# Kernel tuning notes

Hardware: AMD Instinct MI355X
Metric: run time of the kernel (lower is better)

Reference implementation:

```python
import jax, jax.numpy as jnp
import numpy as np

K = 3           # spatial kernel size (kernel_size[1]==kernel_size[2])
STRIDE = 1
EPS_BN = 1e-5


def unfold_replicate(t, k=K, stride=STRIDE):
    """t: (b, C, H, W) -> (b, C, k*k, H//stride, W//stride).
    Replicate-padded kxk patches, row-major window order (matches F.pad(replicate)+F.unfold)."""
    b, C, H, W = t.shape
    pad = (k - 1) // 2
    tp = jnp.pad(t, ((0, 0), (0, 0), (pad, pad), (pad, pad)), mode='edge')
    patches = [tp[:, :, di:di + H:stride, dj:dj + W:stride]
               for di in range(k) for dj in range(k)]
    return jnp.stack(patches, axis=2)


def grid_sample_3d(x, grid):
    """Trilinear grid sample, zeros padding, align_corners=True.
    x: (b,c,D,H,W); grid: (b,P,3) normalized (gx,gy,gz) -> (b,c,P)."""
    b, c, D, H, W = x.shape
    ix = (grid[..., 0] + 1.0) * 0.5 * (W - 1)
    iy = (grid[..., 1] + 1.0) * 0.5 * (H - 1)
    iz = (grid[..., 2] + 1.0) * 0.5 * (D - 1)
    x0 = jnp.floor(ix); y0 = jnp.floor(iy); z0 = jnp.floor(iz)
    fx = ix - x0; fy = iy - y0; fz = iz - z0
    x0i = x0.astype(jnp.int32); y0i = y0.astype(jnp.int32); z0i = z0.astype(jnp.int32)
    x_flat = x.reshape(b, c, D * H * W)
    gather = jax.vmap(lambda xf, idx: xf[:, idx])  # (c,N),(P) -> (c,P) per batch
    out = jnp.zeros((b, c, ix.shape[1]), dtype=x.dtype)
    for dz, wz in ((0, 1.0 - fz), (1, fz)):
        zi = z0i + dz
        for dy, wy in ((0, 1.0 - fy), (1, fy)):
            yi = y0i + dy
            for dx, wx in ((0, 1.0 - fx), (1, fx)):
                xi = x0i + dx
                valid = ((zi >= 0) & (zi < D) & (yi >= 0) & (yi < H)
                         & (xi >= 0) & (xi < W))
                idx = (jnp.clip(zi, 0, D - 1) * H + jnp.clip(yi, 0, H - 1)) * W \
                      + jnp.clip(xi, 0, W - 1)
                w = (wz * wy * wx) * valid.astype(x.dtype)
                out = out + w[:, None, :] * gather(x_flat, idx)
    return out


def gca_cost(x, dp, normal, intri):
    b, c, d, H, W = x.shape
    k2 = K * K
    h, w = H // STRIDE, W // STRIDE
    ctr = k2 // 2

    dp_unf = unfold_replicate(dp)        # (b, d, k2, h, w)
    n_unf = unfold_replicate(normal)     # (b, 3, k2, h, w)
    nx, ny, nz = n_unf[:, 0], n_unf[:, 1], n_unf[:, 2]

    fx = intri[:, 0, 0][:, None, None]; fy = intri[:, 1, 1][:, None, None]
    cx = intri[:, 0, 2][:, None, None]; cy = intri[:, 1, 2][:, None, None]
    yg, xg = jnp.meshgrid(jnp.arange(H, dtype=x.dtype),
                          jnp.arange(W, dtype=x.dtype), indexing='ij')
    posx = (xg[None] - cx) / fx          # (b, H, W) normalized camera rays
    posy = (yg[None] - cy) / fy
    pos_unf = unfold_replicate(jnp.stack([posx, posy], axis=1))  # (b,2,k2,h,w)
    pu, pv = pos_unf[:, 0], pos_unf[:, 1]
    pu_c = pu[:, ctr:ctr + 1]; pv_c = pv[:, ctr:ctr + 1]

    num = nx * pu_c + ny * pv_c + nz
    den = nx * pu + ny * pv + nz
    den = jnp.where(jnp.abs(den) < 1e-8, jnp.sign(den) * 1e-8, den)
    wgt = num / den
    wgt = jnp.where(jnp.isfinite(wgt), wgt, 1.0)   # (b, k2, h, w)

    dp_ctr = dp_unf[:, :, ctr]                      # (b, d, h, w)
    dp_prog = wgt[:, None] * dp_ctr[:, :, None]     # (b, d, k2, h, w)
    interval = dp_unf[:, 1] - dp_unf[:, 0]          # (b, k2, h, w)
    z = (dp_prog - dp_unf[:, 0][:, None]) / interval[:, None]  # (b,d,k2,h,w)

    xy = jnp.broadcast_to(jnp.stack([xg, yg], axis=0)[None], (b, 2, H, W))
    xy_unf = unfold_replicate(xy)                   # (b,2,k2,h,w)
    px = jnp.broadcast_to(xy_unf[:, 0][:, None], (b, d, k2, h, w))
    py = jnp.broadcast_to(xy_unf[:, 1][:, None], (b, d, k2, h, w))

    gx = px / ((W - 1) / 2.0) - 1.0
    gy = py / ((H - 1) / 2.0) - 1.0
    gz = z / ((d - 1) / 2.0) - 1.0
    grid = jnp.stack([gx, gy, gz], axis=-1).reshape(b, d * k2 * h * w, 3)

    samp = grid_sample_3d(x, grid)                  # (b, c, d*k2*h*w)
    samp = samp.reshape(b, c, d, k2, h, w).transpose(0, 1, 3, 2, 4, 5)
    return samp.reshape(b, c * k2, d, h, w)


def reference(x, dp, normal, intri, weight, gamma, beta):
    cost = gca_cost(x, dp, normal, intri)
    y = jax.lax.conv_general_dilated(
        cost, weight, window_strides=(1, 1, 1),
        padding=[(1, 1), (0, 0), (0, 0)],
        dimension_numbers=('NCDHW', 'OIDHW', 'NCDHW'))
    # BatchNorm3d (training-mode batch stats, biased var, eps=1e-5) + ReLU
    mean = jnp.mean(y, axis=(0, 2, 3, 4), keepdims=True)
    var = jnp.var(y, axis=(0, 2, 3, 4), keepdims=True)
    g = gamma.reshape(1, -1, 1, 1, 1)
    bta = beta.reshape(1, -1, 1, 1, 1)
    return jax.nn.relu(g * (y - mean) * jax.lax.rsqrt(var + EPS_BN) + bta)


def setup_inputs() -> dict:
    key = jax.random.key(0)
    ks = jax.random.split(key, 6)
    b, c, d, H, W = 1, 8, 32, 128, 128
    out_ch = 16
    x = jax.random.normal(ks[0], (b, c, d, H, W), dtype=jnp.float32)
    # monotone depth hypotheses per pixel (interval = dp[:,1]-dp[:,0] must be nonzero)
    planes = 425.0 + 10.0 * jnp.arange(d, dtype=jnp.float32)
    scale = 1.0 + 0.05 * jax.random.uniform(ks[1], (b, 1, H, W), dtype=jnp.float32)
    dp = planes[None, :, None, None] * scale                    # (b, d, H, W)
    # near-frontal unit normals so plane-homography weights stay well-conditioned
    nxy = 0.2 * jax.random.normal(ks[2], (b, 2, H, W), dtype=jnp.float32)
    nz = 1.0 + 0.1 * jax.random.normal(ks[3], (b, 1, H, W), dtype=jnp.float32)
    n = jnp.concatenate([nxy, nz], axis=1)
    normal = n / jnp.linalg.norm(n, axis=1, keepdims=True)
    intri = jnp.broadcast_to(
        jnp.array([[1100.0, 0.0, W / 2.0],
                   [0.0, 1100.0, H / 2.0],
                   [0.0, 0.0, 1.0]], dtype=jnp.float32), (b, 3, 3))
    weight = 0.05 * jax.random.normal(ks[4], (out_ch, c * K * K, 3, 1, 1),
                                      dtype=jnp.float32)
    gamma = jnp.ones((out_ch,), jnp.float32)
    beta = jnp.zeros((out_ch,), jnp.float32)
    return {"x": x, "dp": dp, "normal": normal, "intri": intri,
            "weight": weight, "gamma": gamma, "beta": beta}
```

## Files before the change

### kernel.cpp

```cpp
#include <hip/hip_runtime.h>
#include <math.h>

#define W_    128
#define H_    128
#define HW    16384
#define D_    32
#define C_IN  8
#define OC    16
#define NRED  524288.0f

#define SXS   36
#define SXB   1948
#define TILE  2568

typedef __attribute__((ext_vector_type(8))) short bf16x8;
typedef __attribute__((ext_vector_type(4))) float f32x4;

union FragU { uint4 u; bf16x8 h; };


__device__ __forceinline__ unsigned bf16rne(float f) {
    unsigned u = __float_as_uint(f);
    return (u + 0x7fffu + ((u >> 16) & 1u)) >> 16;
}

__device__ __forceinline__ void init_ws(int t, const float* __restrict__ wsrc,
                                        float* __restrict__ ws) {
    if (t < 32) ws[t] = 0.f;
    uint4* af = reinterpret_cast<uint4*>(ws + 64);
    for (int e = t; e < 768; e += 256) {
        int lane = e & 63, pkd = e >> 6;
        int p = pkd / 3, kd = pkd - p * 3;
        int o = lane & 15, kg = lane >> 4;
        int ch = 2 * p + (kg >> 1);
        int jb = (kg & 1) * 8;
        unsigned dw[4];
#pragma unroll
        for (int r2 = 0; r2 < 4; ++r2) {
            int j0 = jb + 2 * r2, j1 = j0 + 1;
            unsigned b0 = (j0 < 9) ? bf16rne(wsrc[(o * 72 + ch * 9 + j0) * 3 + kd]) : 0u;
            unsigned b1 = (j1 < 9) ? bf16rne(wsrc[(o * 72 + ch * 9 + j1) * 3 + kd]) : 0u;
            dw[r2] = b0 | (b1 << 16);
        }
        af[e] = make_uint4(dw[0], dw[1], dw[2], dw[3]);
    }
}

__global__ __launch_bounds__(256) void k_init(const float* __restrict__ wsrc,
                                              float* __restrict__ ws) {
    init_ws((int)threadIdx.x, wsrc, ws);
}

__global__ __launch_bounds__(256) void k_transpose(const float* __restrict__ x,
                                                   float* __restrict__ xt,
                                                   const float* __restrict__ wsrc,
                                                   float* __restrict__ ws) {
    __shared__ float tile[32 * 132];
    int bid = blockIdx.x;
    int c  = bid >> 7;
    int ry = bid & 127;
    int t  = threadIdx.x;
    if (bid == 0) init_ws(t, wsrc, ws);
    const float* src = x + c * (D_ * HW) + ry * W_;
    for (int k = 0; k < 4; ++k) {
        int e  = t * 4 + k * 1024;
        int z  = e >> 7;
        int rx = e & 127;
        float4 v = *reinterpret_cast<const float4*>(src + z * HW + rx);
        *reinterpret_cast<float4*>(&tile[z * 132 + rx]) = v;
    }
    __syncthreads();
    int rx = t >> 1;
    int zh = (t & 1) * 16;
    float* dst = xt + ((size_t)(c * HW + ry * W_ + rx)) * D_ + zh;
    for (int i = 0; i < 4; ++i) {
        float4 v;
        v.x = tile[(zh + i * 4 + 0) * 132 + rx];
        v.y = tile[(zh + i * 4 + 1) * 132 + rx];
        v.z = tile[(zh + i * 4 + 2) * 132 + rx];
        v.w = tile[(zh + i * 4 + 3) * 132 + rx];
        *reinterpret_cast<float4*>(dst + i * 4) = v;
    }
}

template <bool XT, bool YBF>
__global__ __launch_bounds__(512, 4) void k_main(const float* __restrict__ x,
                                                 const float* __restrict__ xt,
                                                 const float* __restrict__ dp,
                                                 const float* __restrict__ nrm,
                                                 const float* __restrict__ intri,
                                                 const uint4* __restrict__ afr,
                                                 float* __restrict__ out,
                                                 unsigned* __restrict__ ybf,
                                                 float* __restrict__ stats) {
    __shared__ float s_pool[2 * SXB];
    __shared__ float s_B[2 * TILE];
    __shared__ float s_wgt[144], s_dp0[144], s_inv[144];
    __shared__ float s_red[64];

    int t   = threadIdx.x;
    int bid = blockIdx.x;
    int r_row = bid >> 3;
    int rx0   = (bid & 7) * 16;

    int seg = t / 144;
    int f   = t - seg * 144;
    int spx = f >> 3;
    int zq  = f & 7;
    int srow = min(max(r_row + seg - 1, 0), H_ - 1);
    int scol = min(max(rx0 - 1 + spx, 0), W_ - 1);
    const float* gsrc     = xt + ((size_t)(srow * W_ + scol)) * D_ + zq * 4;
    const float* gsrc_raw = x + (srow * W_ + scol) + (size_t)(zq * 4) * HW;
    int sdst = 4 + (seg * 18 + spx) * SXS + zq * 4;

    float4 sv;
    if (t < 432) {
        if (XT) {
            sv = *reinterpret_cast<const float4*>(gsrc);
        } else {
            sv.x = gsrc_raw[0]; sv.y = gsrc_raw[HW];
            sv.z = gsrc_raw[2 * HW]; sv.w = gsrc_raw[3 * HW];
        }
    }

    if (t < 144) {
        int p = t / 9, j = t - p * 9;
        int jd = j / 3;
        int dy = jd - 1, dx = (j - jd * 3) - 1;
        int cpix = rx0 + p;
        int ry  = min(max(r_row + dy, 0), H_ - 1);
        int rxn = min(max(cpix + dx, 0), W_ - 1);
        int nb  = ry * W_ + rxn;
        float fx = intri[0], cx = intri[2], fy = intri[4], cy = intri[5];
        float nx = nrm[nb], ny = nrm[HW + nb], nz = nrm[2 * HW + nb];
        float pu  = ((float)rxn  - cx) / fx;
        float pv  = ((float)ry   - cy) / fy;
        float puc = ((float)cpix - cx) / fx;
        float pvc = ((float)r_row - cy) / fy;
        float num = nx * puc + ny * pvc + nz;
        float den = nx * pu + ny * pv + nz;
        if (fabsf(den) < 1e-8f)
            den = (den > 0.f) ? 1e-8f : ((den < 0.f) ? -1e-8f : 0.f);
        float w = num / den;
        if (!isfinite(w)) w = 1.0f;
        float d0  = dp[nb];
        float itv = dp[HW + nb] - d0;
        s_wgt[t] = w;
        s_dp0[t] = d0;
        s_inv[t] = 1.0f / itv;
    }
    if (t < 440) {
        int b  = t / 220;
        int rm = t - b * 220;
        int off = (rm < 4) ? rm : (4 + ((rm - 4) >> 2) * SXS + 32 + ((rm - 4) & 3));
        s_pool[b * SXB + off] = 0.f;
    }
    if (t < 16) s_B[2560 + (t >> 3) * TILE + (t & 7)] = 0.f;
    __syncthreads();
    if (t < 432) *reinterpret_cast<float4*>(&s_pool[sdst]) = sv;

    int px = t & 15;
    int d  = t >> 4;
    float dpv = dp[d * HW + r_row * W_ + rx0 + px];

    int   idx[9];
    float fza[9];
#pragma unroll
    for (int j = 0; j < 9; ++j) {
        int pj = px * 9 + j;
        int jd = j / 3;
        int jx = j - jd * 3;
        float z   = (s_wgt[pj] * dpv - s_dp0[pj]) * s_inv[pj];
        float zc  = fminf(fmaxf(z, -2.0f), 34.0f);
        float z0f = floorf(zc);
        fza[j] = zc - z0f;
        idx[j] = (jd * 18 + px + jx) * SXS + (int)z0f;
    }
    __syncthreads();

    f32x4 acc0 = {0.f, 0.f, 0.f, 0.f};
    f32x4 acc1 = {0.f, 0.f, 0.f, 0.f};
    f32x4 acc2 = {0.f, 0.f, 0.f, 0.f};
    f32x4 acc3 = {0.f, 0.f, 0.f, 0.f};

    int lane = t & 63;
    int wid  = t >> 6;
    int wb   = wid * 4;
    int grp  = lane >> 4;
    unsigned* sBu = reinterpret_cast<unsigned*>(s_B);
    int wrow = (d * 16 + px) * 5;

    for (int c = 0; c < C_IN; ++c) {
        if (c < 7 && t < 432) {
            if (XT) {
                sv = *reinterpret_cast<const float4*>(gsrc + (size_t)(c + 1) * (HW * D_));
            } else {
                const float* b = gsrc_raw + (size_t)(c + 1) * (D_ * HW);
                sv.x = b[0]; sv.y = b[HW]; sv.z = b[2 * HW]; sv.w = b[3 * HW];
            }
        }
        const float* sxp = &s_pool[(c & 1) * SXB + 4];
        float cj[9];
#pragma unroll
        for (int j = 0; j < 9; ++j) {
            float a = sxp[idx[j]];
            float b = sxp[idx[j] + 1];
            cj[j] = fmaf(fza[j], b - a, a);
        }
        unsigned dwv[5];
#pragma unroll
        for (int r2 = 0; r2 < 4; ++r2) {
            asm("v_cvt_pk_bf16_f32 %0, %1, %2"
                : "=v"(dwv[r2]) : "v"(cj[2 * r2]), "v"(cj[2 * r2 + 1]));
        }
        {
            float zz = 0.f;
            asm("v_cvt_pk_bf16_f32 %0, %1, %2"
                : "=v"(dwv[4]) : "v"(cj[8]), "v"(zz));
        }
        {
            int wo = wrow + (c & 1) * TILE;
            sBu[wo + 0] = dwv[0];
            sBu[wo + 1] = dwv[1];
            sBu[wo + 2] = dwv[2];
            sBu[wo + 3] = dwv[3];
            sBu[wo + 4] = dwv[4];
        }
        if (c < 7 && t < 432) *reinterpret_cast<float4*>(&s_pool[((c + 1) & 1) * SXB + sdst]) = sv;
        __syncthreads();

        if (c & 1) {
            int p = c >> 1;
            FragU a0, a1, a2;
            a0.u = afr[(p * 3 + 0) * 64 + lane];
            a1.u = afr[(p * 3 + 1) * 64 + lane];
            a2.u = afr[(p * 3 + 2) * 64 + lane];
            int boff = ((grp & 1) ? 4 : 0) + ((grp >> 1) ? TILE : 0);
#pragma unroll
            for (int q = 0; q < 6; ++q) {
                int db = wb - 1 + q;
                if (db < 0 || db > 31) continue;
                FragU bf;
                int base = (db * 16 + px) * 5 + boff;
                bf.u.x = sBu[base + 0];
                bf.u.y = sBu[base + 1];
                bf.u.z = sBu[base + 2];
                bf.u.w = sBu[base + 3];
                if (q - 0 >= 0 && q - 0 < 4)
                    *(q == 0 ? &acc0 : q == 1 ? &acc1 : q == 2 ? &acc2 : &acc3) =
                        __builtin_amdgcn_mfma_f32_16x16x32_bf16(a0.h, bf.h,
                            *(q == 0 ? &acc0 : q == 1 ? &acc1 : q == 2 ? &acc2 : &acc3), 0, 0, 0);
                if (q - 1 >= 0 && q - 1 < 4)
                    *(q == 1 ? &acc0 : q == 2 ? &acc1 : q == 3 ? &acc2 : &acc3) =
                        __builtin_amdgcn_mfma_f32_16x16x32_bf16(a1.h, bf.h,
                            *(q == 1 ? &acc0 : q == 2 ? &acc1 : q == 3 ? &acc2 : &acc3), 0, 0, 0);
                if (q - 2 >= 0 && q - 2 < 4)
                    *(q == 2 ? &acc0 : q == 3 ? &acc1 : q == 4 ? &acc2 : &acc3) =
                        __builtin_amdgcn_mfma_f32_16x16x32_bf16(a2.h, bf.h,
                            *(q == 2 ? &acc0 : q == 3 ? &acc1 : q == 4 ? &acc2 : &acc3), 0, 0, 0);
            }
            __syncthreads();
        }
    }

    float* s_b = s_pool;
    float bns[4], bnq[4];
    int o_l = t >> 7;
    int dd  = (t >> 2) & 31;
    int q4  = t & 3;
#pragma unroll
    for (int oo = 0; oo < 4; ++oo) {
        if (grp == oo) {
#pragma unroll
            for (int r2 = 0; r2 < 4; ++r2) {
                s_b[(r2 * 32 + wb + 0) * 17 + px] = acc0[r2];
                s_b[(r2 * 32 + wb + 1) * 17 + px] = acc1[r2];
                s_b[(r2 * 32 + wb + 2) * 17 + px] = acc2[r2];
                s_b[(r2 * 32 + wb + 3) * 17 + px] = acc3[r2];
            }
        }
        __syncthreads();
        const float* brow = &s_b[(o_l * 32 + dd) * 17 + q4 * 4];
        float4 yv;
        yv.x = brow[0]; yv.y = brow[1]; yv.z = brow[2]; yv.w = brow[3];
        int o = oo * 4 + o_l;
        size_t base = (size_t)(o * 32 + dd) * HW + r_row * W_ + rx0 + q4 * 4;
        if (YBF) {
            unsigned dA, dB;
            asm("v_cvt_pk_bf16_f32 %0, %1, %2" : "=v"(dA) : "v"(yv.x), "v"(yv.y));
            asm("v_cvt_pk_bf16_f32 %0, %1, %2" : "=v"(dB) : "v"(yv.z), "v"(yv.w));
            uint2 wv; wv.x = dA; wv.y = dB;
            reinterpret_cast<uint2*>(ybf)[base >> 2] = wv;
        } else {
            *reinterpret_cast<float4*>(out + base) = yv;
        }
        bns[oo] = yv.x + yv.y + yv.z + yv.w;
        bnq[oo] = yv.x * yv.x + yv.y * yv.y + yv.z * yv.z + yv.w * yv.w;
        __syncthreads();
    }

#pragma unroll
    for (int oo = 0; oo < 4; ++oo) {
        float s = bns[oo], sq = bnq[oo];
#pragma unroll
        for (int m = 1; m < 64; m <<= 1) {
            s  += __shfl_xor(s, m, 64);
            sq += __shfl_xor(sq, m, 64);
        }
        if ((t & 63) == 0) {
            int w = t >> 6;
            s_red[w * 4 + oo]      = s;
            s_red[32 + w * 4 + oo] = sq;
        }
    }
    __syncthreads();
    if (t < 32) {
        int o  = t & 15;
        int oo = o >> 2, wh = o & 3;
        if (t < 16) {
            float s = s_red[(2 * wh) * 4 + oo] + s_red[(2 * wh + 1) * 4 + oo];
            atomicAdd(&stats[o], s);
        } else {
            float sq = s_red[32 + (2 * wh) * 4 + oo] + s_red[32 + (2 * wh + 1) * 4 + oo];
            atomicAdd(&stats[16 + o], sq);
        }
    }
}

template <bool YBF>
__global__ __launch_bounds__(256) void k_bn(float* __restrict__ out,
                                            const unsigned* __restrict__ ybf,
                                            const float* __restrict__ stats,
                                            const float* __restrict__ gamma,
                                            const float* __restrict__ beta) {
    int i4 = blockIdx.x * 256 + threadIdx.x;
    int o  = i4 >> 17;
    float invN = 1.f / NRED;
    float mean = stats[o] * invN;
    float var  = stats[16 + o] * invN - mean * mean;
    float rstd = rsqrtf(var + 1e-5f);
    float a = gamma[o] * rstd;
    float b = beta[o] - mean * a;
    float4 y;
    if (YBF) {
        uint2 v = reinterpret_cast<const uint2*>(ybf)[i4];
        y.x = __uint_as_float(v.x << 16);
        y.y = __uint_as_float(v.x & 0xffff0000u);
        y.z = __uint_as_float(v.y << 16);
        y.w = __uint_as_float(v.y & 0xffff0000u);
    } else {
        y = reinterpret_cast<float4*>(out)[i4];
    }
    y.x = fmaxf(0.f, fmaf(y.x, a, b));
    y.y = fmaxf(0.f, fmaf(y.y, a, b));
    y.z = fmaxf(0.f, fmaf(y.z, a, b));
    y.w = fmaxf(0.f, fmaf(y.w, a, b));
    reinterpret_cast<float4*>(out)[i4] = y;
}

extern "C" void kernel_launch(void* const* d_in, const int* in_sizes, int n_in,
                              void* d_out, int out_size, void* d_ws, size_t ws_size,
                              hipStream_t stream) {
    const float* x     = (const float*)d_in[0];
    const float* dp    = (const float*)d_in[1];
    const float* nrm   = (const float*)d_in[2];
    const float* intri = (const float*)d_in[3];
    const float* wsrc  = (const float*)d_in[4];
    const float* gamma = (const float*)d_in[5];
    const float* beta  = (const float*)d_in[6];
    float* out = (float*)d_out;
    float* ws  = (float*)d_ws;

    bool xt_ok = ws_size >= (size_t)(8192 + 4194304) * 4;
    bool yb_ok = ws_size >= (size_t)(8192 + 4194304 + 4194304) * 4;
    float* xt = ws + 8192;
    unsigned* ybf = (unsigned*)(ws + 8192 + 4194304);
    const uint4* afr = (const uint4*)(ws + 64);

    if (xt_ok) {
        hipLaunchKernelGGL(k_transpose, dim3(1024), dim3(256), 0, stream, x, xt, wsrc, ws);
        if (yb_ok) {
            hipLaunchKernelGGL((k_main<true, true>), dim3(1024), dim3(512), 0, stream,
                               x, xt, dp, nrm, intri, afr, out, ybf, ws);
            hipLaunchKernelGGL(k_bn<true>, dim3(8192), dim3(256), 0, stream,
                               out, ybf, ws, gamma, beta);
        } else {
            hipLaunchKernelGGL((k_main<true, false>), dim3(1024), dim3(512), 0, stream,
                               x, xt, dp, nrm, intri, afr, out, ybf, ws);
            hipLaunchKernelGGL(k_bn<false>, dim3(8192), dim3(256), 0, stream,
                               out, ybf, ws, gamma, beta);
        }
    } else {
        hipLaunchKernelGGL(k_init, dim3(1), dim3(256), 0, stream, wsrc, ws);
        hipLaunchKernelGGL((k_main<false, false>), dim3(1024), dim3(512), 0, stream,
                           x, xt, dp, nrm, intri, afr, out, ybf, ws);
        hipLaunchKernelGGL(k_bn<false>, dim3(8192), dim3(256), 0, stream,
                           out, ybf, ws, gamma, beta);
    }
}
```

Measured before the change: 61.84 us.

## Drop x transpose pre-pass and gather directly from original layout

Removes the k_transpose kernel that rewrote x into a depth-contiguous layout. k_main now always loads the four depth values per thread with strided scalar reads from the original layout, and a tiny k_init kernel prepares the weight fragments. This saves a full read and write pass over x plus one launch, but the main kernel's loads become four strided scalar accesses instead of one float4. It also lowers the workspace needed for the bf16 intermediate path.

```diff
diff --git a/kernel.cpp b/kernel.cpp
--- a/kernel.cpp
+++ b/kernel.cpp
@@ -24,8 +24,9 @@
     return (u + 0x7fffu + ((u >> 16) & 1u)) >> 16;
 }
 
-__device__ __forceinline__ void init_ws(int t, const float* __restrict__ wsrc,
-                                        float* __restrict__ ws) {
+__global__ __launch_bounds__(256) void k_init(const float* __restrict__ wsrc,
+                                              float* __restrict__ ws) {
+    int t = threadIdx.x;
     if (t < 32) ws[t] = 0.f;
     uint4* af = reinterpret_cast<uint4*>(ws + 64);
     for (int e = t; e < 768; e += 256) {
@@ -46,46 +47,8 @@
     }
 }
 
-__global__ __launch_bounds__(256) void k_init(const float* __restrict__ wsrc,
-                                              float* __restrict__ ws) {
-    init_ws((int)threadIdx.x, wsrc, ws);
-}
-
-__global__ __launch_bounds__(256) void k_transpose(const float* __restrict__ x,
-                                                   float* __restrict__ xt,
-                                                   const float* __restrict__ wsrc,
-                                                   float* __restrict__ ws) {
-    __shared__ float tile[32 * 132];
-    int bid = blockIdx.x;
-    int c  = bid >> 7;
-    int ry = bid & 127;
-    int t  = threadIdx.x;
-    if (bid == 0) init_ws(t, wsrc, ws);
-    const float* src = x + c * (D_ * HW) + ry * W_;
-    for (int k = 0; k < 4; ++k) {
-        int e  = t * 4 + k * 1024;
-        int z  = e >> 7;
-        int rx = e & 127;
-        float4 v = *reinterpret_cast<const float4*>(src + z * HW + rx);
-        *reinterpret_cast<float4*>(&tile[z * 132 + rx]) = v;
-    }
-    __syncthreads();
-    int rx = t >> 1;
-    int zh = (t & 1) * 16;
-    float* dst = xt + ((size_t)(c * HW + ry * W_ + rx)) * D_ + zh;
-    for (int i = 0; i < 4; ++i) {
-        float4 v;
-        v.x = tile[(zh + i * 4 + 0) * 132 + rx];
-        v.y = tile[(zh + i * 4 + 1) * 132 + rx];
-        v.z = tile[(zh + i * 4 + 2) * 132 + rx];
-        v.w = tile[(zh + i * 4 + 3) * 132 + rx];
-        *reinterpret_cast<float4*>(dst + i * 4) = v;
-    }
-}
-
-template <bool XT, bool YBF>
+template <bool YBF>
 __global__ __launch_bounds__(512, 4) void k_main(const float* __restrict__ x,
-                                                 const float* __restrict__ xt,
                                                  const float* __restrict__ dp,
                                                  const float* __restrict__ nrm,
                                                  const float* __restrict__ intri,
@@ -109,18 +72,13 @@
     int zq  = f & 7;
     int srow = min(max(r_row + seg - 1, 0), H_ - 1);
     int scol = min(max(rx0 - 1 + spx, 0), W_ - 1);
-    const float* gsrc     = xt + ((size_t)(srow * W_ + scol)) * D_ + zq * 4;
     const float* gsrc_raw = x + (srow * W_ + scol) + (size_t)(zq * 4) * HW;
     int sdst = 4 + (seg * 18 + spx) * SXS + zq * 4;
 
     float4 sv;
     if (t < 432) {
-        if (XT) {
-            sv = *reinterpret_cast<const float4*>(gsrc);
-        } else {
-            sv.x = gsrc_raw[0]; sv.y = gsrc_raw[HW];
-            sv.z = gsrc_raw[2 * HW]; sv.w = gsrc_raw[3 * HW];
-        }
+        sv.x = gsrc_raw[0]; sv.y = gsrc_raw[HW];
+        sv.z = gsrc_raw[2 * HW]; sv.w = gsrc_raw[3 * HW];
     }
 
     if (t < 144) {
@@ -192,12 +150,8 @@
 
     for (int c = 0; c < C_IN; ++c) {
         if (c < 7 && t < 432) {
-            if (XT) {
-                sv = *reinterpret_cast<const float4*>(gsrc + (size_t)(c + 1) * (HW * D_));
-            } else {
-                const float* b = gsrc_raw + (size_t)(c + 1) * (D_ * HW);
-                sv.x = b[0]; sv.y = b[HW]; sv.z = b[2 * HW]; sv.w = b[3 * HW];
-            }
+            const float* b = gsrc_raw + (size_t)(c + 1) * (D_ * HW);
+            sv.x = b[0]; sv.y = b[HW]; sv.z = b[2 * HW]; sv.w = b[3 * HW];
         }
         const float* sxp = &s_pool[(c & 1) * SXB + 4];
         float cj[9];
@@ -371,29 +325,19 @@
     float* out = (float*)d_out;
     float* ws  = (float*)d_ws;
 
-    bool xt_ok = ws_size >= (size_t)(8192 + 4194304) * 4;
-    bool yb_ok = ws_size >= (size_t)(8192 + 4194304 + 4194304) * 4;
-    float* xt = ws + 8192;
-    unsigned* ybf = (unsigned*)(ws + 8192 + 4194304);
+    bool yb_ok = ws_size >= (size_t)(8192 + 4194304) * 4;
+    unsigned* ybf = (unsigned*)(ws + 8192);
     const uint4* afr = (const uint4*)(ws + 64);
 
-    if (xt_ok) {
-        hipLaunchKernelGGL(k_transpose, dim3(1024), dim3(256), 0, stream, x, xt, wsrc, ws);
-        if (yb_ok) {
-            hipLaunchKernelGGL((k_main<true, true>), dim3(1024), dim3(512), 0, stream,
-                               x, xt, dp, nrm, intri, afr, out, ybf, ws);
-            hipLaunchKernelGGL(k_bn<true>, dim3(8192), dim3(256), 0, stream,
-                               out, ybf, ws, gamma, beta);
-        } else {
-            hipLaunchKernelGGL((k_main<true, false>), dim3(1024), dim3(512), 0, stream,
-                               x, xt, dp, nrm, intri, afr, out, ybf, ws);
-            hipLaunchKernelGGL(k_bn<false>, dim3(8192), dim3(256), 0, stream,
-                               out, ybf, ws, gamma, beta);
-        }
+    hipLaunchKernelGGL(k_init, dim3(1), dim3(256), 0, stream, wsrc, ws);
+    if (yb_ok) {
+        hipLaunchKernelGGL(k_main<true>, dim3(1024), dim3(512), 0, stream,
+                           x, dp, nrm, intri, afr, out, ybf, ws);
+        hipLaunchKernelGGL(k_bn<true>, dim3(8192), dim3(256), 0, stream,
+                           out, ybf, ws, gamma, beta);
     } else {
-        hipLaunchKernelGGL(k_init, dim3(1), dim3(256), 0, stream, wsrc, ws);
-        hipLaunchKernelGGL((k_main<false, false>), dim3(1024), dim3(512), 0, stream,
-                           x, xt, dp, nrm, intri, afr, out, ybf, ws);
+        hipLaunchKernelGGL(k_main<false>, dim3(1024), dim3(512), 0, stream,
+                           x, dp, nrm, intri, afr, out, ybf, ws);
         hipLaunchKernelGGL(k_bn<false>, dim3(8192), dim3(256), 0, stream,
                            out, ybf, ws, gamma, beta);
     }
```

Result: faster. 59.06 us (-4.5%).

## Store transposed input volume as bf16 and sample from packed bf16 shared pool

Applied to the files above, without the earlier changes.

The transpose kernel now writes the depth-contiguous copy of x as packed bf16 pairs instead of fp32, which halves that intermediate's write and read traffic. The main kernel stages the volume in a smaller packed-bf16 shared pool and unpacks the right half-word for each trilinear tap using a parity bit stored in the index. The fp32 input path is split into a separate kernel. This lowers global and LDS traffic and LDS footprint at the cost of extra bit-manipulation ALU work and bf16 rounding of the sampled volume before interpolation.

```diff
diff --git a/kernel.cpp b/kernel.cpp
--- a/kernel.cpp
+++ b/kernel.cpp
@@ -9,6 +9,8 @@
 #define OC    16
 #define NRED  524288.0f
 
+#define SXS2  19
+#define SXB2  1028
 #define SXS   36
 #define SXB   1948
 #define TILE  2568
@@ -52,7 +54,7 @@
 }
 
 __global__ __launch_bounds__(256) void k_transpose(const float* __restrict__ x,
-                                                   float* __restrict__ xt,
+                                                   unsigned* __restrict__ xtb,
                                                    const float* __restrict__ wsrc,
                                                    float* __restrict__ ws) {
     __shared__ float tile[32 * 132];
@@ -72,28 +74,26 @@
     __syncthreads();
     int rx = t >> 1;
     int zh = (t & 1) * 16;
-    float* dst = xt + ((size_t)(c * HW + ry * W_ + rx)) * D_ + zh;
-    for (int i = 0; i < 4; ++i) {
-        float4 v;
-        v.x = tile[(zh + i * 4 + 0) * 132 + rx];
-        v.y = tile[(zh + i * 4 + 1) * 132 + rx];
-        v.z = tile[(zh + i * 4 + 2) * 132 + rx];
-        v.w = tile[(zh + i * 4 + 3) * 132 + rx];
-        *reinterpret_cast<float4*>(dst + i * 4) = v;
-    }
-}
-
-template <bool XT, bool YBF>
-__global__ __launch_bounds__(512, 4) void k_main(const float* __restrict__ x,
-                                                 const float* __restrict__ xt,
-                                                 const float* __restrict__ dp,
-                                                 const float* __restrict__ nrm,
-                                                 const float* __restrict__ intri,
-                                                 const uint4* __restrict__ afr,
-                                                 float* __restrict__ out,
-                                                 unsigned* __restrict__ ybf,
-                                                 float* __restrict__ stats) {
-    __shared__ float s_pool[2 * SXB];
+    unsigned dw[8];
+#pragma unroll
+    for (int i = 0; i < 8; ++i) {
+        float lo = tile[(zh + 2 * i) * 132 + rx];
+        float hi = tile[(zh + 2 * i + 1) * 132 + rx];
+        asm("v_cvt_pk_bf16_f32 %0, %1, %2" : "=v"(dw[i]) : "v"(lo), "v"(hi));
+    }
+    unsigned* dst = xtb + (size_t)(c * HW + ry * W_ + rx) * 16 + (t & 1) * 8;
+    reinterpret_cast<uint4*>(dst)[0] = make_uint4(dw[0], dw[1], dw[2], dw[3]);
+    reinterpret_cast<uint4*>(dst)[1] = make_uint4(dw[4], dw[5], dw[6], dw[7]);
+}
+
+__global__ __launch_bounds__(512, 4) void k_main_bf(const unsigned* __restrict__ xtb,
+                                                    const float* __restrict__ dp,
+                                                    const float* __restrict__ nrm,
+                                                    const float* __restrict__ intri,
+                                                    const uint4* __restrict__ afr,
+                                                    unsigned* __restrict__ ybf,
+                                                    float* __restrict__ stats) {
+    __shared__ unsigned s_poolU[2 * SXB2];
     __shared__ float s_B[2 * TILE];
     __shared__ float s_wgt[144], s_dp0[144], s_inv[144];
     __shared__ float s_red[64];
@@ -109,19 +109,12 @@
     int zq  = f & 7;
     int srow = min(max(r_row + seg - 1, 0), H_ - 1);
     int scol = min(max(rx0 - 1 + spx, 0), W_ - 1);
-    const float* gsrc     = xt + ((size_t)(srow * W_ + scol)) * D_ + zq * 4;
-    const float* gsrc_raw = x + (srow * W_ + scol) + (size_t)(zq * 4) * HW;
-    int sdst = 4 + (seg * 18 + spx) * SXS + zq * 4;
-
-    float4 sv;
-    if (t < 432) {
-        if (XT) {
-            sv = *reinterpret_cast<const float4*>(gsrc);
-        } else {
-            sv.x = gsrc_raw[0]; sv.y = gsrc_raw[HW];
-            sv.z = gsrc_raw[2 * HW]; sv.w = gsrc_raw[3 * HW];
-        }
-    }
+    const unsigned* gsrcU = xtb + (size_t)(srow * W_ + scol) * 16 + zq * 2;
+    int colL = seg * 18 + spx;
+    int sdst = colL * SXS2 + 1 + 2 * zq;
+
+    uint2 sv;
+    if (t < 432) sv = *reinterpret_cast<const uint2*>(gsrcU);
 
     if (t < 144) {
         int p = t / 9, j = t - p * 9;
@@ -149,21 +142,25 @@
         s_dp0[t] = d0;
         s_inv[t] = 1.0f / itv;
     }
-    if (t < 440) {
-        int b  = t / 220;
-        int rm = t - b * 220;
-        int off = (rm < 4) ? rm : (4 + ((rm - 4) >> 2) * SXS + 32 + ((rm - 4) & 3));
-        s_pool[b * SXB + off] = 0.f;
+    if (t < 324) {
+        int b  = t / 162;
+        int rm = t - b * 162;
+        int col = rm / 3, w3 = rm - col * 3;
+        int off = col * SXS2 + ((w3 == 0) ? 0 : (16 + w3));
+        s_poolU[b * SXB2 + off] = 0u;
     }
     if (t < 16) s_B[2560 + (t >> 3) * TILE + (t & 7)] = 0.f;
     __syncthreads();
-    if (t < 432) *reinterpret_cast<float4*>(&s_pool[sdst]) = sv;
+    if (t < 432) {
+        s_poolU[sdst]     = sv.x;
+        s_poolU[sdst + 1] = sv.y;
+    }
 
     int px = t & 15;
     int d  = t >> 4;
     float dpv = dp[d * HW + r_row * W_ + rx0 + px];
 
-    int   idx[9];
+    unsigned idq[9];
     float fza[9];
 #pragma unroll
     for (int j = 0; j < 9; ++j) {
@@ -174,7 +171,9 @@
         float zc  = fminf(fmaxf(z, -2.0f), 34.0f);
         float z0f = floorf(zc);
         fza[j] = zc - z0f;
-        idx[j] = (jd * 18 + px + jx) * SXS + (int)z0f;
+        int s0 = 2 + (int)z0f;
+        idq[j] = (unsigned)((jd * 18 + px + jx) * SXS2 + (s0 >> 1))
+               | ((unsigned)(s0 & 1) << 16);
     }
     __syncthreads();
 
@@ -191,20 +190,19 @@
     int wrow = (d * 16 + px) * 5;
 
     for (int c = 0; c < C_IN; ++c) {
-        if (c < 7 && t < 432) {
-            if (XT) {
-                sv = *reinterpret_cast<const float4*>(gsrc + (size_t)(c + 1) * (HW * D_));
-            } else {
-                const float* b = gsrc_raw + (size_t)(c + 1) * (D_ * HW);
-                sv.x = b[0]; sv.y = b[HW]; sv.z = b[2 * HW]; sv.w = b[3 * HW];
-            }
-        }
-        const float* sxp = &s_pool[(c & 1) * SXB + 4];
+        if (c < 7 && t < 432)
+            sv = *reinterpret_cast<const uint2*>(gsrcU + (size_t)(c + 1) * (HW * 16));
+        const unsigned* PU = s_poolU + (c & 1) * SXB2;
         float cj[9];
 #pragma unroll
         for (int j = 0; j < 9; ++j) {
-            float a = sxp[idx[j]];
-            float b = sxp[idx[j] + 1];
+            unsigned v = idq[j];
+            unsigned q = v & 0xffffu;
+            unsigned p = v >> 16;
+            unsigned u0 = PU[q];
+            unsigned u1 = PU[q + p];
+            float a = __uint_as_float(p ? (u0 & 0xffff0000u) : (u0 << 16));
+            float b = __uint_as_float(p ? (u1 << 16) : (u0 & 0xffff0000u));
             cj[j] = fmaf(fza[j], b - a, a);
         }
         unsigned dwv[5];
@@ -226,7 +224,11 @@
             sBu[wo + 3] = dwv[3];
             sBu[wo + 4] = dwv[4];
         }
-        if (c < 7 && t < 432) *reinterpret_cast<float4*>(&s_pool[((c + 1) & 1) * SXB + sdst]) = sv;
+        if (c < 7 && t < 432) {
+            int ds2 = ((c + 1) & 1) * SXB2 + sdst;
+            s_poolU[ds2]     = sv.x;
+            s_poolU[ds2 + 1] = sv.y;
+        }
         __syncthreads();
 
         if (c & 1) {
@@ -263,7 +265,7 @@
         }
     }
 
-    float* s_b = s_pool;
+    float* s_b = s_B;
     float bns[4], bnq[4];
     int o_l = t >> 7;
     int dd  = (t >> 2) & 31;
@@ -285,15 +287,235 @@
         yv.x = brow[0]; yv.y = brow[1]; yv.z = brow[2]; yv.w = brow[3];
         int o = oo * 4 + o_l;
         size_t base = (size_t)(o * 32 + dd) * HW + r_row * W_ + rx0 + q4 * 4;
-        if (YBF) {
-            unsigned dA, dB;
-            asm("v_cvt_pk_bf16_f32 %0, %1, %2" : "=v"(dA) : "v"(yv.x), "v"(yv.y));
-            asm("v_cvt_pk_bf16_f32 %0, %1, %2" : "=v"(dB) : "v"(yv.z), "v"(yv.w));
-            uint2 wv; wv.x = dA; wv.y = dB;
-            reinterpret_cast<uint2*>(ybf)[base >> 2] = wv;
+        unsigned dA, dB;
+        asm("v_cvt_pk_bf16_f32 %0, %1, %2" : "=v"(dA) : "v"(yv.x), "v"(yv.y));
+        asm("v_cvt_pk_bf16_f32 %0, %1, %2" : "=v"(dB) : "v"(yv.z), "v"(yv.w));
+        uint2 wv; wv.x = dA; wv.y = dB;
+        reinterpret_cast<uint2*>(ybf)[base >> 2] = wv;
+        bns[oo] = yv.x + yv.y + yv.z + yv.w;
+        bnq[oo] = yv.x * yv.x + yv.y * yv.y + yv.z * yv.z + yv.w * yv.w;
+        __syncthreads();
+    }
+
+#pragma unroll
+    for (int oo = 0; oo < 4; ++oo) {
+        float s = bns[oo], sq = bnq[oo];
+#pragma unroll
+        for (int m = 1; m < 64; m <<= 1) {
+            s  += __shfl_xor(s, m, 64);
+            sq += __shfl_xor(sq, m, 64);
+        }
+        if ((t & 63) == 0) {
+            int w = t >> 6;
+            s_red[w * 4 + oo]      = s;
+            s_red[32 + w * 4 + oo] = sq;
+        }
+    }
+    __syncthreads();
+    if (t < 32) {
+        int o  = t & 15;
+        int oo = o >> 2, wh = o & 3;
+        if (t < 16) {
+            float s = s_red[(2 * wh) * 4 + oo] + s_red[(2 * wh + 1) * 4 + oo];
+            atomicAdd(&stats[o], s);
         } else {
-            *reinterpret_cast<float4*>(out + base) = yv;
-        }
+            float sq = s_red[32 + (2 * wh) * 4 + oo] + s_red[32 + (2 * wh + 1) * 4 + oo];
+            atomicAdd(&stats[16 + o], sq);
+        }
+    }
+}
+
+__global__ __launch_bounds__(512, 4) void k_main_raw(const float* __restrict__ x,
+                                                     const float* __restrict__ dp,
+                                                     const float* __restrict__ nrm,
+                                                     const float* __restrict__ intri,
+                                                     const uint4* __restrict__ afr,
+                                                     float* __restrict__ out,
+                                                     float* __restrict__ stats) {
+    __shared__ float s_pool[2 * SXB];
+    __shared__ float s_B[2 * TILE];
+    __shared__ float s_wgt[144], s_dp0[144], s_inv[144];
+    __shared__ float s_red[64];
+
+    int t   = threadIdx.x;
+    int bid = blockIdx.x;
+    int r_row = bid >> 3;
+    int rx0   = (bid & 7) * 16;
+
+    int seg = t / 144;
+    int f   = t - seg * 144;
+    int spx = f >> 3;
+    int zq  = f & 7;
+    int srow = min(max(r_row + seg - 1, 0), H_ - 1);
+    int scol = min(max(rx0 - 1 + spx, 0), W_ - 1);
+    const float* gsrc_raw = x + (srow * W_ + scol) + (size_t)(zq * 4) * HW;
+    int sdst = 4 + (seg * 18 + spx) * SXS + zq * 4;
+
+    float4 sv;
+    if (t < 432) {
+        sv.x = gsrc_raw[0]; sv.y = gsrc_raw[HW];
+        sv.z = gsrc_raw[2 * HW]; sv.w = gsrc_raw[3 * HW];
+    }
+
+    if (t < 144) {
+        int p = t / 9, j = t - p * 9;
+        int jd = j / 3;
+        int dy = jd - 1, dx = (j - jd * 3) - 1;
+        int cpix = rx0 + p;
+        int ry  = min(max(r_row + dy, 0), H_ - 1);
+        int rxn = min(max(cpix + dx, 0), W_ - 1);
+        int nb  = ry * W_ + rxn;
+        float fx = intri[0], cx = intri[2], fy = intri[4], cy = intri[5];
+        float nx = nrm[nb], ny = nrm[HW + nb], nz = nrm[2 * HW + nb];
+        float pu  = ((float)rxn  - cx) / fx;
+        float pv  = ((float)ry   - cy) / fy;
+        float puc = ((float)cpix - cx) / fx;
+        float pvc = ((float)r_row - cy) / fy;
+        float num = nx * puc + ny * pvc + nz;
+        float den = nx * pu + ny * pv + nz;
+        if (fabsf(den) < 1e-8f)
+            den = (den > 0.f) ? 1e-8f : ((den < 0.f) ? -1e-8f : 0.f);
+        float w = num / den;
+        if (!isfinite(w)) w = 1.0f;
+        float d0  = dp[nb];
+        float itv = dp[HW + nb] - d0;
+        s_wgt[t] = w;
+        s_dp0[t] = d0;
+        s_inv[t] = 1.0f / itv;
+    }
+    if (t < 440) {
+        int b  = t / 220;
+        int rm = t - b * 220;
+        int off = (rm < 4) ? rm : (4 + ((rm - 4) >> 2) * SXS + 32 + ((rm - 4) & 3));
+        s_pool[b * SXB + off] = 0.f;
+    }
+    if (t < 16) s_B[2560 + (t >> 3) * TILE + (t & 7)] = 0.f;
+    __syncthreads();
+    if (t < 432) *reinterpret_cast<float4*>(&s_pool[sdst]) = sv;
+
+    int px = t & 15;
+    int d  = t >> 4;
+    float dpv = dp[d * HW + r_row * W_ + rx0 + px];
+
+    int   idx[9];
+    float fza[9];
+#pragma unroll
+    for (int j = 0; j < 9; ++j) {
+        int pj = px * 9 + j;
+        int jd = j / 3;
+        int jx = j - jd * 3;
+        float z   = (s_wgt[pj] * dpv - s_dp0[pj]) * s_inv[pj];
+        float zc  = fminf(fmaxf(z, -2.0f), 34.0f);
+        float z0f = floorf(zc);
+        fza[j] = zc - z0f;
+        idx[j] = (jd * 18 + px + jx) * SXS + (int)z0f;
+    }
+    __syncthreads();
+
+    f32x4 acc0 = {0.f, 0.f, 0.f, 0.f};
+    f32x4 acc1 = {0.f, 0.f, 0.f, 0.f};
+    f32x4 acc2 = {0.f, 0.f, 0.f, 0.f};
+    f32x4 acc3 = {0.f, 0.f, 0.f, 0.f};
+
+    int lane = t & 63;
+    int wid  = t >> 6;
+    int wb   = wid * 4;
+    int grp  = lane >> 4;
+    unsigned* sBu = reinterpret_cast<unsigned*>(s_B);
+    int wrow = (d * 16 + px) * 5;
+
+    for (int c = 0; c < C_IN; ++c) {
+        if (c < 7 && t < 432) {
+            const float* b = gsrc_raw + (size_t)(c + 1) * (D_ * HW);
+            sv.x = b[0]; sv.y = b[HW]; sv.z = b[2 * HW]; sv.w = b[3 * HW];
+        }
+        const float* sxp = &s_pool[(c & 1) * SXB + 4];
+        float cj[9];
+#pragma unroll
+        for (int j = 0; j < 9; ++j) {
+            float a = sxp[idx[j]];
+            float b = sxp[idx[j] + 1];
+            cj[j] = fmaf(fza[j], b - a, a);
+        }
+        unsigned dwv[5];
+#pragma unroll
+        for (int r2 = 0; r2 < 4; ++r2) {
+            asm("v_cvt_pk_bf16_f32 %0, %1, %2"
+                : "=v"(dwv[r2]) : "v"(cj[2 * r2]), "v"(cj[2 * r2 + 1]));
+        }
+        {
+            float zz = 0.f;
+            asm("v_cvt_pk_bf16_f32 %0, %1, %2"
+                : "=v"(dwv[4]) : "v"(cj[8]), "v"(zz));
+        }
+        {
+            int wo = wrow + (c & 1) * TILE;
+            sBu[wo + 0] = dwv[0];
+            sBu[wo + 1] = dwv[1];
+            sBu[wo + 2] = dwv[2];
+            sBu[wo + 3] = dwv[3];
+            sBu[wo + 4] = dwv[4];
+        }
+        if (c < 7 && t < 432) *reinterpret_cast<float4*>(&s_pool[((c + 1) & 1) * SXB + sdst]) = sv;
+        __syncthreads();
+
+        if (c & 1) {
+            int p = c >> 1;
+            FragU a0, a1, a2;
+            a0.u = afr[(p * 3 + 0) * 64 + lane];
+            a1.u = afr[(p * 3 + 1) * 64 + lane];
+            a2.u = afr[(p * 3 + 2) * 64 + lane];
+            int boff = ((grp & 1) ? 4 : 0) + ((grp >> 1) ? TILE : 0);
+#pragma unroll
+            for (int q = 0; q < 6; ++q) {
+                int db = wb - 1 + q;
+                if (db < 0 || db > 31) continue;
+                FragU bf;
+                int base = (db * 16 + px) * 5 + boff;
+                bf.u.x = sBu[base + 0];
+                bf.u.y = sBu[base + 1];
+                bf.u.z = sBu[base + 2];
+                bf.u.w = sBu[base + 3];
+                if (q - 0 >= 0 && q - 0 < 4)
+                    *(q == 0 ? &acc0 : q == 1 ? &acc1 : q == 2 ? &acc2 : &acc3) =
+                        __builtin_amdgcn_mfma_f32_16x16x32_bf16(a0.h, bf.h,
+                            *(q == 0 ? &acc0 : q == 1 ? &acc1 : q == 2 ? &acc2 : &acc3), 0, 0, 0);
+                if (q - 1 >= 0 && q - 1 < 4)
+                    *(q == 1 ? &acc0 : q == 2 ? &acc1 : q == 3 ? &acc2 : &acc3) =
+                        __builtin_amdgcn_mfma_f32_16x16x32_bf16(a1.h, bf.h,
+                            *(q == 1 ? &acc0 : q == 2 ? &acc1 : q == 3 ? &acc2 : &acc3), 0, 0, 0);
+                if (q - 2 >= 0 && q - 2 < 4)
+                    *(q == 2 ? &acc0 : q == 3 ? &acc1 : q == 4 ? &acc2 : &acc3) =
+                        __builtin_amdgcn_mfma_f32_16x16x32_bf16(a2.h, bf.h,
+                            *(q == 2 ? &acc0 : q == 3 ? &acc1 : q == 4 ? &acc2 : &acc3), 0, 0, 0);
+            }
+            __syncthreads();
+        }
+    }
+
+    float* s_b = s_pool;
+    float bns[4], bnq[4];
+    int o_l = t >> 7;
+    int dd  = (t >> 2) & 31;
+    int q4  = t & 3;
+#pragma unroll
+    for (int oo = 0; oo < 4; ++oo) {
+        if (grp == oo) {
+#pragma unroll
+            for (int r2 = 0; r2 < 4; ++r2) {
+                s_b[(r2 * 32 + wb + 0) * 17 + px] = acc0[r2];
+                s_b[(r2 * 32 + wb + 1) * 17 + px] = acc1[r2];
+                s_b[(r2 * 32 + wb + 2) * 17 + px] = acc2[r2];
+                s_b[(r2 * 32 + wb + 3) * 17 + px] = acc3[r2];
+            }
+        }
+        __syncthreads();
+        const float* brow = &s_b[(o_l * 32 + dd) * 17 + q4 * 4];
+        float4 yv;
+        yv.x = brow[0]; yv.y = brow[1]; yv.z = brow[2]; yv.w = brow[3];
+        int o = oo * 4 + o_l;
+        size_t base = (size_t)(o * 32 + dd) * HW + r_row * W_ + rx0 + q4 * 4;
+        *reinterpret_cast<float4*>(out + base) = yv;
         bns[oo] = yv.x + yv.y + yv.z + yv.w;
         bnq[oo] = yv.x * yv.x + yv.y * yv.y + yv.z * yv.z + yv.w * yv.w;
         __syncthreads();
@@ -371,29 +593,21 @@
     float* out = (float*)d_out;
     float* ws  = (float*)d_ws;
 
-    bool xt_ok = ws_size >= (size_t)(8192 + 4194304) * 4;
-    bool yb_ok = ws_size >= (size_t)(8192 + 4194304 + 4194304) * 4;
-    float* xt = ws + 8192;
-    unsigned* ybf = (unsigned*)(ws + 8192 + 4194304);
+    bool ok = ws_size >= (size_t)(8192 + 2097152 + 4194304) * 4;
+    unsigned* xtb = (unsigned*)(ws + 8192);
+    unsigned* ybf = (unsigned*)(ws + 8192 + 2097152);
     const uint4* afr = (const uint4*)(ws + 64);
 
-    if (xt_ok) {
-        hipLaunchKernelGGL(k_transpose, dim3(1024), dim3(256), 0, stream, x, xt, wsrc, ws);
-        if (yb_ok) {
-            hipLaunchKernelGGL((k_main<true, true>), dim3(1024), dim3(512), 0, stream,
-                               x, xt, dp, nrm, intri, afr, out, ybf, ws);
-            hipLaunchKernelGGL(k_bn<true>, dim3(8192), dim3(256), 0, stream,
-                               out, ybf, ws, gamma, beta);
-        } else {
-            hipLaunchKernelGGL((k_main<true, false>), dim3(1024), dim3(512), 0, stream,
-                               x, xt, dp, nrm, intri, afr, out, ybf, ws);
-            hipLaunchKernelGGL(k_bn<false>, dim3(8192), dim3(256), 0, stream,
-                               out, ybf, ws, gamma, beta);
-        }
+    if (ok) {
+        hipLaunchKernelGGL(k_transpose, dim3(1024), dim3(256), 0, stream, x, xtb, wsrc, ws);
+        hipLaunchKernelGGL(k_main_bf, dim3(1024), dim3(512), 0, stream,
+                           xtb, dp, nrm, intri, afr, ybf, ws);
+        hipLaunchKernelGGL(k_bn<true>, dim3(8192), dim3(256), 0, stream,
+                           out, ybf, ws, gamma, beta);
     } else {
         hipLaunchKernelGGL(k_init, dim3(1), dim3(256), 0, stream, wsrc, ws);
-        hipLaunchKernelGGL((k_main<false, false>), dim3(1024), dim3(512), 0, stream,
-                           x, xt, dp, nrm, intri, afr, out, ybf, ws);
+        hipLaunchKernelGGL(k_main_raw, dim3(1024), dim3(512), 0, stream,
+                           x, dp, nrm, intri, afr, out, ws);
         hipLaunchKernelGGL(k_bn<false>, dim3(8192), dim3(256), 0, stream,
                            out, ybf, ws, gamma, beta);
     }
```

Result: faster. 59.26 us (-4.2%).
